# Kernel optimization log

Hardware: AMD Instinct MI355X
Metric: run time of the kernel (lower is better)

## Reference

```python
import jax, jax.numpy as jnp
import numpy as np

N = 50000   # nodes
E = 800000  # edges
D = 256     # input_dim == hidden_dim (required by original code path)
O = 32      # output_dim
ALPHA = 0.5      # APPNP teleport
ALPHA_RES = 0.0  # residual mix on output
BETA = 1.0       # neighbor-aggregation scale
EPS = 1e-12


def _l2norm(h):
    # F.normalize(h, p=2, dim=1)
    n = jnp.sqrt(jnp.sum(h * h, axis=1, keepdims=True))
    return h / jnp.maximum(n, EPS)


def _gappnp(x, row, col):
    # GAPPNP with K=1, symmetric normalization, self-loops (APPNP-style step)
    sl = jnp.arange(N, dtype=row.dtype)
    r = jnp.concatenate([row, sl])
    c = jnp.concatenate([col, sl])
    deg = jax.ops.segment_sum(jnp.ones(r.shape, x.dtype), r, num_segments=N)
    dinv = jnp.where(deg > 0, jax.lax.rsqrt(jnp.maximum(deg, 1.0)), 0.0)
    norm = dinv[r] * dinv[c]                      # [E+N]
    agg = jax.ops.segment_sum(norm[:, None] * x[c], r, num_segments=N)  # [N, D]
    h = (1.0 - ALPHA) * BETA * agg + ALPHA * x
    return (1.0 - ALPHA_RES) * h + ALPHA_RES * x


def setup_inputs() -> dict:
    key = jax.random.key(0)
    ks = jax.random.split(key, 8)
    s = 1.0 / np.sqrt(D)
    return {
        "x": jax.random.normal(ks[0], (N, D), dtype=jnp.float32),
        "edge_index": jax.random.randint(ks[1], (2, E), 0, N, dtype=jnp.int32),
        "W0": jax.random.normal(ks[2], (D, D), dtype=jnp.float32) * s,
        "b0": jnp.zeros((D,), jnp.float32),
        "Wn0": jax.random.normal(ks[3], (D, D), dtype=jnp.float32) * s,
        "bn0": jnp.zeros((D,), jnp.float32),
        "W1": jax.random.normal(ks[4], (D, D), dtype=jnp.float32) * s,
        "b1": jnp.zeros((D,), jnp.float32),
        "Wn1": jax.random.normal(ks[5], (D, D), dtype=jnp.float32) * s,
        "bn1": jnp.zeros((D,), jnp.float32),
        "W2": jax.random.normal(ks[6], (D, O), dtype=jnp.float32) * s,
        "b2": jnp.zeros((O,), jnp.float32),
    }


def reference(x, edge_index, W0, b0, Wn0, bn0, W1, b1, Wn1, bn1, W2, b2):
    # eval mode: dropout is identity
    row, col = edge_index[0], edge_index[1]
    h = x
    for (W, b, Wn, bn) in ((W0, b0, Wn0, bn0), (W1, b1, Wn1, bn1)):
        h = h @ W + b                       # fc[c]
        nb = h @ Wn + bn                    # fc_n[c] (separate_neighbors)
        nb = _gappnp(nb, row, col)          # propagate neighbors
        h = h + nb
        h = _l2norm(h)                      # norm == 'normalize'
        h = jax.nn.relu(h)                  # activation 'relu'
    h = h @ W2 + b2                         # final layer, no norm (c != 0)
    return h
```

## Files before the change

### kernel.cpp

```cpp
#include <hip/hip_runtime.h>
#include <hip/hip_bf16.h>

#define NN 50000
#define NE 800000
#define DD 256
#define OO 32

typedef __attribute__((ext_vector_type(8))) short short8;
typedef __attribute__((ext_vector_type(4))) float float4v;

#define AS1 __attribute__((address_space(1)))
#define AS3 __attribute__((address_space(3)))

__device__ __forceinline__ float lo16f(unsigned int u) {
    union { unsigned int i; float f; } x; x.i = u << 16; return x.f;
}
__device__ __forceinline__ float hi16f(unsigned int u) {
    union { unsigned int i; float f; } x; x.i = u & 0xFFFF0000u; return x.f;
}
__device__ __forceinline__ unsigned short f2b(float f) {
    union { float f; unsigned int i; } x;
    x.f = f;
    unsigned int r = x.i + 0x7FFFu + ((x.i >> 16) & 1u);
    return (unsigned short)(r >> 16);
}

__global__ void count_kernel(const int* __restrict__ row, int* __restrict__ cnt, int E) {
    int e = blockIdx.x * blockDim.x + threadIdx.x;
    if (e < E) atomicAdd(&cnt[row[e]], 1);
}

__global__ __launch_bounds__(256) void block_sums(const int* __restrict__ cnt,
                                                  int* __restrict__ bsum, int N) {
    __shared__ int s[256];
    int idx = blockIdx.x * 256 + threadIdx.x;
    s[threadIdx.x] = (idx < N) ? cnt[idx] : 0;
    __syncthreads();
    for (int o = 128; o > 0; o >>= 1) {
        if (threadIdx.x < o) s[threadIdx.x] += s[threadIdx.x + o];
        __syncthreads();
    }
    if (threadIdx.x == 0) bsum[blockIdx.x] = s[0];
}

__global__ __launch_bounds__(256) void scan_bsums(const int* __restrict__ bsum,
                                                  int* __restrict__ bpre, int nb) {
    __shared__ int s[256];
    int t = threadIdx.x;
    int v0 = (t < nb) ? bsum[t] : 0;
    s[t] = v0;
    __syncthreads();
    for (int o = 1; o < 256; o <<= 1) {
        int v = (t >= o) ? s[t - o] : 0;
        __syncthreads();
        s[t] += v;
        __syncthreads();
    }
    if (t < nb) bpre[t] = s[t] - v0;
}

__global__ __launch_bounds__(256) void fill_rowptr(const int* __restrict__ cnt,
                                                   const int* __restrict__ bpre,
                                                   int* __restrict__ row_ptr,
                                                   int* __restrict__ cursor,
                                                   float* __restrict__ dinv, int N, int E) {
    __shared__ int s[256];
    int t = threadIdx.x;
    int idx = blockIdx.x * 256 + t;
    int c = (idx < N) ? cnt[idx] : 0;
    s[t] = c;
    __syncthreads();
    for (int o = 1; o < 256; o <<= 1) {
        int v = (t >= o) ? s[t - o] : 0;
        __syncthreads();
        s[t] += v;
        __syncthreads();
    }
    int excl = bpre[blockIdx.x] + s[t] - c;
    if (idx < N) {
        row_ptr[idx] = excl;
        cursor[idx] = excl;
        dinv[idx] = rsqrtf((float)(c + 1));
    }
    if (idx == N) row_ptr[N] = E;
}

__global__ __launch_bounds__(256) void touch_csr(const uint4* __restrict__ t, int n16) {
    int slice = blockIdx.x >> 3;
    int per = (n16 + 31) >> 5;
    int base = slice * per;
    int end = base + per; if (end > n16) end = n16;
    unsigned int sx = 0, sy = 0, sz = 0, sw = 0;
    for (int i = base + threadIdx.x; i < end; i += 256) {
        uint4 v = t[i];
        sx ^= v.x; sy ^= v.y; sz ^= v.z; sw ^= v.w;
    }
    asm volatile("" :: "v"(sx), "v"(sy), "v"(sz), "v"(sw));
}

__global__ void scatter_kernel(const int* __restrict__ row, const int* __restrict__ col,
                               int* __restrict__ cursor,
                               unsigned short* __restrict__ csr_col, int E) {
    int e = blockIdx.x * blockDim.x + threadIdx.x;
    if (e < E) {
        int p = atomicAdd(&cursor[row[e]], 1);
        csr_col[p] = (unsigned short)col[e];
    }
}

__global__ __launch_bounds__(256) void cast_x_kernel(const float* __restrict__ x,
                                                     unsigned short* __restrict__ xb, int n4) {
    int i = blockIdx.x * 256 + threadIdx.x;
    if (i < n4) {
        float4 v = ((const float4*)x)[i];
        ushort4 o;
        o.x = f2b(v.x); o.y = f2b(v.y); o.z = f2b(v.z); o.w = f2b(v.w);
        ((ushort4*)xb)[i] = o;
    }
}

__device__ __forceinline__ int pack_idx(int k, int n) {
    return (k >> 5) * 8192 + (n >> 4) * 512 + (((k & 31) >> 3) * 16 + (n & 15)) * 8 + (k & 7);
}

__global__ __launch_bounds__(256) void cast_pack_w(const float* __restrict__ W0,
                                                   const float* __restrict__ W1,
                                                   const float* __restrict__ W2,
                                                   unsigned short* __restrict__ Wp0,
                                                   unsigned short* __restrict__ Wp1,
                                                   unsigned short* __restrict__ Wt2) {
    int n = blockIdx.x, k = threadIdx.x;
    if (blockIdx.y == 0) Wp0[pack_idx(k, n)] = f2b(W0[k * 256 + n]);
    else if (blockIdx.y == 1) Wp1[pack_idx(k, n)] = f2b(W1[k * 256 + n]);
    else if (n < 32) Wt2[n * 256 + k] = f2b(W2[k * 32 + n]);
}

__global__ __launch_bounds__(256) void compose_wc(const float* __restrict__ W0,
                                                  const float* __restrict__ Wn0,
                                                  const float* __restrict__ W1,
                                                  const float* __restrict__ Wn1,
                                                  unsigned short* __restrict__ Wp0,
                                                  unsigned short* __restrict__ Wp1) {
    const float* W  = blockIdx.y ? W1 : W0;
    const float* Wn = blockIdx.y ? Wn1 : Wn0;
    unsigned short* T = blockIdx.y ? Wp1 : Wp0;
    __shared__ float wrow[256];
    int k = blockIdx.x, n = threadIdx.x;
    wrow[n] = W[k * 256 + n];
    __syncthreads();
    float s = 0.f;
#pragma unroll 8
    for (int m = 0; m < 256; ++m) s = fmaf(wrow[m], Wn[m * 256 + n], s);
    T[pack_idx(k + 256, n)] = f2b(s);
}

__global__ __launch_bounds__(256) void compose_bc(const float* __restrict__ b0_,
                                                  const float* __restrict__ Wn0,
                                                  const float* __restrict__ bn0,
                                                  const float* __restrict__ b1_,
                                                  const float* __restrict__ Wn1,
                                                  const float* __restrict__ bn1,
                                                  float* __restrict__ bc0,
                                                  float* __restrict__ bc1) {
    const float* b  = blockIdx.y ? b1_ : b0_;
    const float* Wn = blockIdx.y ? Wn1 : Wn0;
    const float* bn = blockIdx.y ? bn1 : bn0;
    float* bc = blockIdx.y ? bc1 : bc0;
    int n = threadIdx.x;
    float s = bn[n];
    for (int m = 0; m < 256; ++m) s = fmaf(b[m], Wn[m * 256 + n], s);
    bc[n] = s;
}

__global__ __launch_bounds__(256) void agg_g(const unsigned short* __restrict__ A,
                                             const float* __restrict__ dinv,
                                             const int* __restrict__ row_ptr,
                                             const unsigned short* __restrict__ csr_col,
                                             unsigned short* __restrict__ G,
                                             float* __restrict__ pv) {
    int wave = threadIdx.x >> 6, lane = threadIdx.x & 63;
    int half = lane >> 5, s = lane & 31;
    int v = blockIdx.x * 4 + wave;
    float dv = dinv[v];
    const uint4* A4 = (const uint4*)A;

    float a0 = 0.f, a1 = 0.f, a2 = 0.f, a3 = 0.f;
    float a4 = 0.f, a5 = 0.f, a6 = 0.f, a7 = 0.f;
    float sdc = 0.f;

    int st = row_ptr[v], en = row_ptr[v + 1];
    for (int b0 = st; b0 < en; b0 += 64) {
        int mm = en - b0;
        if (mm > 64) mm = 64;
        int c = 0;
        float dc = 0.f;
        if (lane < mm) { c = csr_col[b0 + lane]; dc = dinv[c]; }
        sdc += dc;
        int pairs4 = (((mm + 1) >> 1) + 3) & ~3;
        for (int j = 0; j < pairs4; j += 4) {
            int ci[4];
            float di[4];
            uint4 u[4];
#pragma unroll
            for (int q = 0; q < 4; ++q) {
                int srcl = 2 * (j + q) + half;
                ci[q] = __shfl(c, srcl);
                di[q] = __shfl(dc, srcl);
            }
#pragma unroll
            for (int q = 0; q < 4; ++q) u[q] = A4[(size_t)ci[q] * 32 + s];
#pragma unroll
            for (int q = 0; q < 4; ++q) {
                a0 = fmaf(di[q], lo16f(u[q].x), a0);
                a1 = fmaf(di[q], hi16f(u[q].x), a1);
                a2 = fmaf(di[q], lo16f(u[q].y), a2);
                a3 = fmaf(di[q], hi16f(u[q].y), a3);
                a4 = fmaf(di[q], lo16f(u[q].z), a4);
                a5 = fmaf(di[q], hi16f(u[q].z), a5);
                a6 = fmaf(di[q], lo16f(u[q].w), a6);
                a7 = fmaf(di[q], hi16f(u[q].w), a7);
            }
        }
    }
    a0 += __shfl_xor(a0, 32); a1 += __shfl_xor(a1, 32);
    a2 += __shfl_xor(a2, 32); a3 += __shfl_xor(a3, 32);
    a4 += __shfl_xor(a4, 32); a5 += __shfl_xor(a5, 32);
    a6 += __shfl_xor(a6, 32); a7 += __shfl_xor(a7, 32);
#pragma unroll
    for (int o = 32; o > 0; o >>= 1) sdc += __shfl_xor(sdc, o);

    if (half == 0) {
        uint4 au = A4[(size_t)v * 32 + s];
        float av[8] = {lo16f(au.x), hi16f(au.x), lo16f(au.y), hi16f(au.y),
                       lo16f(au.z), hi16f(au.z), lo16f(au.w), hi16f(au.w)};
        float aa[8] = {a0, a1, a2, a3, a4, a5, a6, a7};
        unsigned short ov[8];
#pragma unroll
        for (int i = 0; i < 8; ++i)
            ov[i] = f2b(0.5f * dv * (dv * av[i] + aa[i]) + 0.5f * av[i]);
        *(short8*)&G[(size_t)v * 256 + s * 8] = *(short8*)ov;
    }
    if (lane == 0) pv[v] = 0.5f * dv * (dv + sdc) + 0.5f;
}

__global__ __launch_bounds__(256, 2) void gemm512_norm(const unsigned short* __restrict__ A,
                                                       const unsigned short* __restrict__ G,
                                                       const unsigned short* __restrict__ Wp,
                                                       const float* __restrict__ bias,
                                                       const float* __restrict__ biasc,
                                                       const float* __restrict__ pv,
                                                       unsigned short* __restrict__ Out,
                                                       int M) {
    __shared__ unsigned short smem[16384];
    int tid = threadIdx.x, lane = tid & 63, wave = tid >> 6;
    int fr = lane & 15, quad = lane >> 4, fk = quad * 8;
    int rb = blockIdx.x * 128;

    int r0 = rb + wave * 32 + fr;      if (r0 >= M) r0 = M - 1;
    int r1 = rb + wave * 32 + 16 + fr; if (r1 >= M) r1 = M - 1;
    const unsigned short* ap0 = A + (size_t)r0 * 256 + fk;
    const unsigned short* ap1 = A + (size_t)r1 * 256 + fk;
    const unsigned short* gp0 = G + (size_t)r0 * 256 + fk;
    const unsigned short* gp1 = G + (size_t)r1 * 256 + fk;

    float4v acc[2][16];
#pragma unroll
    for (int i = 0; i < 2; ++i)
#pragma unroll
        for (int j = 0; j < 16; ++j) acc[i][j] = (float4v){0.f, 0.f, 0.f, 0.f};

#pragma unroll
    for (int i = 0; i < 4; ++i) {
        int ch = wave * 4 + i;
        __builtin_amdgcn_global_load_lds((const AS1 void*)(Wp + ch * 512 + lane * 8),
                                         (AS3 void*)&smem[ch * 512], 16, 0, 0);
    }
    short8 a0c = *(const short8*)ap0;
    short8 a1c = *(const short8*)ap1;

    for (int kk = 0; kk < 16; ++kk) {
        __syncthreads();
        int cur = (kk & 1) * 8192;
        if (kk < 15) {
            int nxt = ((kk + 1) & 1) * 8192;
#pragma unroll
            for (int i = 0; i < 4; ++i) {
                int ch = wave * 4 + i;
                __builtin_amdgcn_global_load_lds(
                    (const AS1 void*)(Wp + (kk + 1) * 8192 + ch * 512 + lane * 8),
                    (AS3 void*)&smem[nxt + ch * 512], 16, 0, 0);
            }
        }
        short8 a0n, a1n;
        if (kk < 15) {
            int kn = kk + 1;
            a0n = (kn < 8) ? *(const short8*)(ap0 + kn * 32) : *(const short8*)(gp0 + (kn - 8) * 32);
            a1n = (kn < 8) ? *(const short8*)(ap1 + kn * 32) : *(const short8*)(gp1 + (kn - 8) * 32);
        }
#pragma unroll
        for (int j = 0; j < 16; ++j) {
            short8 b = *(const short8*)&smem[cur + j * 512 + lane * 8];
            acc[0][j] = __builtin_amdgcn_mfma_f32_16x16x32_bf16(a0c, b, acc[0][j], 0, 0, 0);
            acc[1][j] = __builtin_amdgcn_mfma_f32_16x16x32_bf16(a1c, b, acc[1][j], 0, 0, 0);
        }
        a0c = a0n;
        a1c = a1n;
    }

    float bv[16], bcv[16];
#pragma unroll
    for (int j = 0; j < 16; ++j) {
        bv[j] = bias[j * 16 + fr];
        bcv[j] = biasc[j * 16 + fr];
    }
    float pvr[2][4];
#pragma unroll
    for (int i = 0; i < 2; ++i)
#pragma unroll
        for (int r = 0; r < 4; ++r) {
            int rg = rb + wave * 32 + i * 16 + quad * 4 + r;
            if (rg >= M) rg = M - 1;
            pvr[i][r] = pv[rg];
        }
    float ss[2][4] = {{0.f, 0.f, 0.f, 0.f}, {0.f, 0.f, 0.f, 0.f}};
#pragma unroll
    for (int i = 0; i < 2; ++i)
#pragma unroll
        for (int j = 0; j < 16; ++j)
#pragma unroll
            for (int r = 0; r < 4; ++r) {
                float t = acc[i][j][r] + bv[j] + pvr[i][r] * bcv[j];
                acc[i][j][r] = t;
                ss[i][r] = fmaf(t, t, ss[i][r]);
            }
#pragma unroll
    for (int o = 1; o < 16; o <<= 1)
#pragma unroll
        for (int i = 0; i < 2; ++i)
#pragma unroll
            for (int r = 0; r < 4; ++r) ss[i][r] += __shfl_xor(ss[i][r], o);
    float inv[2][4];
#pragma unroll
    for (int i = 0; i < 2; ++i)
#pragma unroll
        for (int r = 0; r < 4; ++r) inv[i][r] = 1.0f / fmaxf(sqrtf(ss[i][r]), 1e-12f);

#pragma unroll
    for (int rd = 0; rd < 2; ++rd) {
        __syncthreads();
        if ((wave >> 1) == rd) {
#pragma unroll
            for (int i = 0; i < 2; ++i)
#pragma unroll
                for (int j = 0; j < 16; ++j)
#pragma unroll
                    for (int r = 0; r < 4; ++r)
                        smem[((wave & 1) * 32 + i * 16 + quad * 4 + r) * 256 + j * 16 + fr] =
                            f2b(fmaxf(acc[i][j][r] * inv[i][r], 0.f));
        }
        __syncthreads();
#pragma unroll
        for (int b = 0; b < 8; ++b) {
            int chunk = b * 256 + tid;
            int rw = chunk >> 5, part = chunk & 31;
            int gr = rb + rd * 64 + rw;
            if (gr < M)
                *(short8*)&Out[(size_t)gr * 256 + part * 8] =
                    *(const short8*)&smem[rw * 256 + part * 8];
        }
    }
}

__global__ __launch_bounds__(256) void gemm_final_mfma(const unsigned short* __restrict__ A,
                                                       const unsigned short* __restrict__ Wt2,
                                                       const float* __restrict__ b2,
                                                       float* __restrict__ out, int M) {
    __shared__ unsigned short Als[128 * 32];
    __shared__ unsigned short Bls[32 * 32];
    int tid = threadIdx.x;
    int lane = tid & 63, wave = tid >> 6;
    int rowBase = blockIdx.x * 128;

    float4v acc[2][2];
#pragma unroll
    for (int i = 0; i < 2; ++i)
#pragma unroll
        for (int j = 0; j < 2; ++j) acc[i][j] = (float4v){0.f, 0.f, 0.f, 0.f};

    int sRow = wave * 32 + (lane >> 2);
    int sK = (lane & 3) * 8;
    int fr = lane & 15, fk = (lane >> 4) * 8;
    int bn = tid >> 3, bk4 = (tid & 7) * 4;

    for (int k0 = 0; k0 < 256; k0 += 32) {
        int r0 = rowBase + sRow;       if (r0 >= M) r0 = M - 1;
        int r1 = rowBase + sRow + 16;  if (r1 >= M) r1 = M - 1;
        __builtin_amdgcn_global_load_lds((const AS1 void*)(A + (size_t)r0 * 256 + k0 + sK),
                                         (AS3 void*)&Als[(wave * 32) * 32], 16, 0, 0);
        __builtin_amdgcn_global_load_lds((const AS1 void*)(A + (size_t)r1 * 256 + k0 + sK),
                                         (AS3 void*)&Als[(wave * 32 + 16) * 32], 16, 0, 0);
        *(ushort4*)&Bls[bn * 32 + bk4] = *(const ushort4*)&Wt2[bn * 256 + k0 + bk4];
        __syncthreads();

        short8 af[2], bfr[2];
#pragma unroll
        for (int i = 0; i < 2; ++i)
            af[i] = *(const short8*)&Als[(wave * 32 + i * 16 + fr) * 32 + fk];
#pragma unroll
        for (int j = 0; j < 2; ++j)
            bfr[j] = *(const short8*)&Bls[(j * 16 + fr) * 32 + fk];
#pragma unroll
        for (int i = 0; i < 2; ++i)
#pragma unroll
            for (int j = 0; j < 2; ++j)
                acc[i][j] = __builtin_amdgcn_mfma_f32_16x16x32_bf16(af[i], bfr[j], acc[i][j], 0, 0, 0);
        __syncthreads();
    }

    int cr = (lane >> 4) * 4, cc = lane & 15;
#pragma unroll
    for (int i = 0; i < 2; ++i) {
#pragma unroll
        for (int j = 0; j < 2; ++j) {
            int colg = j * 16 + cc;
            float bv = b2[colg];
#pragma unroll
            for (int r = 0; r < 4; ++r) {
                int rowg = rowBase + wave * 32 + i * 16 + cr + r;
                if (rowg < M) out[(size_t)rowg * 32 + colg] = acc[i][j][r] + bv;
            }
        }
    }
}

extern "C" void kernel_launch(void* const* d_in, const int* in_sizes, int n_in,
                              void* d_out, int out_size, void* d_ws, size_t ws_size,
                              hipStream_t stream) {
    const float* x   = (const float*)d_in[0];
    const int* edge  = (const int*)d_in[1];
    const float* W0  = (const float*)d_in[2];
    const float* b0  = (const float*)d_in[3];
    const float* Wn0 = (const float*)d_in[4];
    const float* bn0 = (const float*)d_in[5];
    const float* W1  = (const float*)d_in[6];
    const float* b1  = (const float*)d_in[7];
    const float* Wn1 = (const float*)d_in[8];
    const float* bn1 = (const float*)d_in[9];
    const float* W2  = (const float*)d_in[10];
    const float* b2  = (const float*)d_in[11];
    float* out = (float*)d_out;

    const int N = NN, E = NE;
    const int* row = edge;
    const int* col = edge + E;

    char* p = (char*)d_ws;
    unsigned short* Xbf = (unsigned short*)p; p += (size_t)N * DD * 2;
    unsigned short* Gbf = (unsigned short*)p; p += (size_t)N * DD * 2;
    unsigned short* Abf = (unsigned short*)p; p += (size_t)N * DD * 2;
    unsigned short* Wp0 = (unsigned short*)p; p += 16 * 8192 * 2;
    unsigned short* Wp1 = (unsigned short*)p; p += 16 * 8192 * 2;
    unsigned short* Wt2 = (unsigned short*)p; p += 32 * 256 * 2;
    float* bc0   = (float*)p; p += 256 * 4;
    float* bc1   = (float*)p; p += 256 * 4;
    float* pv    = (float*)p; p += (size_t)N * 4;
    int* cnt     = (int*)p; p += (size_t)N * 4;
    int* row_ptr = (int*)p; p += (size_t)(N + 4) * 4;
    int* cursor  = (int*)p; p += (size_t)N * 4;
    float* dinv  = (float*)p; p += (size_t)N * 4;
    unsigned short* csr_col = (unsigned short*)p; p += (size_t)E * 2;
    int* bsum    = (int*)p; p += 256 * 4;
    int* bpre    = (int*)p; p += 256 * 4;

    const int nblk = (N + 255) / 256;
    const int eb = (E + 255) / 256;

    hipMemsetAsync(cnt, 0, (size_t)N * sizeof(int), stream);
    count_kernel<<<eb, 256, 0, stream>>>(row, cnt, E);
    block_sums<<<nblk, 256, 0, stream>>>(cnt, bsum, N);
    scan_bsums<<<1, 256, 0, stream>>>(bsum, bpre, nblk);
    fill_rowptr<<<nblk, 256, 0, stream>>>(cnt, bpre, row_ptr, cursor, dinv, N, E);
    touch_csr<<<256, 256, 0, stream>>>((const uint4*)csr_col, E * 2 / 16);
    scatter_kernel<<<eb, 256, 0, stream>>>(row, col, cursor, csr_col, E);

    cast_x_kernel<<<(N * DD / 4 + 255) / 256, 256, 0, stream>>>(x, Xbf, N * DD / 4);
    cast_pack_w<<<dim3(256, 3), 256, 0, stream>>>(W0, W1, W2, Wp0, Wp1, Wt2);
    compose_wc<<<dim3(256, 2), 256, 0, stream>>>(W0, Wn0, W1, Wn1, Wp0, Wp1);
    compose_bc<<<dim3(1, 2), 256, 0, stream>>>(b0, Wn0, bn0, b1, Wn1, bn1, bc0, bc1);

    const int gTiles = (N + 127) / 128;
    agg_g<<<N / 4, 256, 0, stream>>>(Xbf, dinv, row_ptr, csr_col, Gbf, pv);
    gemm512_norm<<<gTiles, 256, 0, stream>>>(Xbf, Gbf, Wp0, b0, bc0, pv, Abf, N);
    agg_g<<<N / 4, 256, 0, stream>>>(Abf, dinv, row_ptr, csr_col, Gbf, pv);
    gemm512_norm<<<gTiles, 256, 0, stream>>>(Abf, Gbf, Wp1, b1, bc1, pv, Xbf, N);
    gemm_final_mfma<<<(N + 127) / 128, 256, 0, stream>>>(Xbf, Wt2, b2, out, N);
}
```

Measured before the change: 390.0 us.

## Fuse neighbor aggregation into the per-layer GEMM via shared-memory G tile

Merges the aggregation kernel and the 512-K GEMM+normalize kernel into one per-layer kernel. Each 512-thread block first aggregates its 128 rows into a swizzled LDS tile, then runs the MFMA GEMM with the first half of K read from global A and the second half read from LDS. This drops the global round trip of the G buffer and one launch per layer. In exchange the weight tile is single-buffered with two barriers per K step, each wave now handles 16 rows instead of 32, and the gather phase cannot overlap the GEMM within a block, so load balance and occupancy become more sensitive to per-block degree.

Result: slower. 400.3 us (+2.6%).

```diff
diff --git a/kernel.cpp b/kernel.cpp
--- a/kernel.cpp
+++ b/kernel.cpp
@@ -172,139 +172,137 @@
     bc[n] = s;
 }
 
-__global__ __launch_bounds__(256) void agg_g(const unsigned short* __restrict__ A,
-                                             const float* __restrict__ dinv,
-                                             const int* __restrict__ row_ptr,
-                                             const unsigned short* __restrict__ csr_col,
-                                             unsigned short* __restrict__ G,
-                                             float* __restrict__ pv) {
-    int wave = threadIdx.x >> 6, lane = threadIdx.x & 63;
+__global__ __launch_bounds__(512, 4) void layer_fused(const unsigned short* __restrict__ A,
+                                                      const float* __restrict__ dinv,
+                                                      const int* __restrict__ row_ptr,
+                                                      const unsigned short* __restrict__ csr_col,
+                                                      const unsigned short* __restrict__ Wp,
+                                                      const float* __restrict__ bias,
+                                                      const float* __restrict__ biasc,
+                                                      float* __restrict__ pv,
+                                                      unsigned short* __restrict__ Out,
+                                                      int M) {
+    __shared__ unsigned short Gt[128 * 256];
+    __shared__ unsigned short Bs[8192];
+    int tid = threadIdx.x, lane = tid & 63, wave = tid >> 6;
     int half = lane >> 5, s = lane & 31;
-    int v = blockIdx.x * 4 + wave;
-    float dv = dinv[v];
+    int rb = blockIdx.x * 128;
+
+    {
+        int ch = wave * 2;
+        __builtin_amdgcn_global_load_lds((const AS1 void*)(Wp + ch * 512 + lane * 8),
+                                         (AS3 void*)&Bs[ch * 512], 16, 0, 0);
+        __builtin_amdgcn_global_load_lds((const AS1 void*)(Wp + (ch + 1) * 512 + lane * 8),
+                                         (AS3 void*)&Bs[(ch + 1) * 512], 16, 0, 0);
+    }
+
     const uint4* A4 = (const uint4*)A;
-
-    float a0 = 0.f, a1 = 0.f, a2 = 0.f, a3 = 0.f;
-    float a4 = 0.f, a5 = 0.f, a6 = 0.f, a7 = 0.f;
-    float sdc = 0.f;
-
-    int st = row_ptr[v], en = row_ptr[v + 1];
-    for (int b0 = st; b0 < en; b0 += 64) {
-        int mm = en - b0;
-        if (mm > 64) mm = 64;
-        int c = 0;
-        float dc = 0.f;
-        if (lane < mm) { c = csr_col[b0 + lane]; dc = dinv[c]; }
-        sdc += dc;
-        int pairs4 = (((mm + 1) >> 1) + 3) & ~3;
-        for (int j = 0; j < pairs4; j += 4) {
-            int ci[4];
-            float di[4];
-            uint4 u[4];
-#pragma unroll
-            for (int q = 0; q < 4; ++q) {
-                int srcl = 2 * (j + q) + half;
-                ci[q] = __shfl(c, srcl);
-                di[q] = __shfl(dc, srcl);
+    int li = rb + wave * 16 + lane; if (li > NN) li = NN;
+    int rpv = (lane < 17) ? row_ptr[li] : 0;
+
+    for (int t = 0; t < 16; ++t) {
+        int v = rb + wave * 16 + t;
+        if (v >= M) break;
+        float dv = dinv[v];
+        int st = __shfl(rpv, t), en = __shfl(rpv, t + 1);
+
+        float a0 = 0.f, a1 = 0.f, a2 = 0.f, a3 = 0.f;
+        float a4 = 0.f, a5 = 0.f, a6 = 0.f, a7 = 0.f;
+        float sdc = 0.f;
+        for (int b0 = st; b0 < en; b0 += 64) {
+            int mm = en - b0;
+            if (mm > 64) mm = 64;
+            int c = 0;
+            float dc = 0.f;
+            if (lane < mm) { c = csr_col[b0 + lane]; dc = dinv[c]; }
+            sdc += dc;
+            int pairs4 = (((mm + 1) >> 1) + 3) & ~3;
+            for (int j = 0; j < pairs4; j += 4) {
+                int ci[4];
+                float di[4];
+                uint4 u[4];
+#pragma unroll
+                for (int q = 0; q < 4; ++q) {
+                    int srcl = 2 * (j + q) + half;
+                    ci[q] = __shfl(c, srcl);
+                    di[q] = __shfl(dc, srcl);
+                }
+#pragma unroll
+                for (int q = 0; q < 4; ++q) u[q] = A4[(size_t)ci[q] * 32 + s];
+#pragma unroll
+                for (int q = 0; q < 4; ++q) {
+                    a0 = fmaf(di[q], lo16f(u[q].x), a0);
+                    a1 = fmaf(di[q], hi16f(u[q].x), a1);
+                    a2 = fmaf(di[q], lo16f(u[q].y), a2);
+                    a3 = fmaf(di[q], hi16f(u[q].y), a3);
+                    a4 = fmaf(di[q], lo16f(u[q].z), a4);
+                    a5 = fmaf(di[q], hi16f(u[q].z), a5);
+                    a6 = fmaf(di[q], lo16f(u[q].w), a6);
+                    a7 = fmaf(di[q], hi16f(u[q].w), a7);
+                }
             }
-#pragma unroll
-            for (int q = 0; q < 4; ++q) u[q] = A4[(size_t)ci[q] * 32 + s];
-#pragma unroll
-            for (int q = 0; q < 4; ++q) {
-                a0 = fmaf(di[q], lo16f(u[q].x), a0);
-                a1 = fmaf(di[q], hi16f(u[q].x), a1);
-                a2 = fmaf(di[q], lo16f(u[q].y), a2);
-                a3 = fmaf(di[q], hi16f(u[q].y), a3);
-                a4 = fmaf(di[q], lo16f(u[q].z), a4);
-                a5 = fmaf(di[q], hi16f(u[q].z), a5);
-                a6 = fmaf(di[q], lo16f(u[q].w), a6);
-                a7 = fmaf(di[q], hi16f(u[q].w), a7);
-            }
-        }
-    }
-    a0 += __shfl_xor(a0, 32); a1 += __shfl_xor(a1, 32);
-    a2 += __shfl_xor(a2, 32); a3 += __shfl_xor(a3, 32);
-    a4 += __shfl_xor(a4, 32); a5 += __shfl_xor(a5, 32);
-    a6 += __shfl_xor(a6, 32); a7 += __shfl_xor(a7, 32);
-#pragma unroll
-    for (int o = 32; o > 0; o >>= 1) sdc += __shfl_xor(sdc, o);
-
-    if (half == 0) {
-        uint4 au = A4[(size_t)v * 32 + s];
-        float av[8] = {lo16f(au.x), hi16f(au.x), lo16f(au.y), hi16f(au.y),
-                       lo16f(au.z), hi16f(au.z), lo16f(au.w), hi16f(au.w)};
-        float aa[8] = {a0, a1, a2, a3, a4, a5, a6, a7};
-        unsigned short ov[8];
-#pragma unroll
-        for (int i = 0; i < 8; ++i)
-            ov[i] = f2b(0.5f * dv * (dv * av[i] + aa[i]) + 0.5f * av[i]);
-        *(short8*)&G[(size_t)v * 256 + s * 8] = *(short8*)ov;
-    }
-    if (lane == 0) pv[v] = 0.5f * dv * (dv + sdc) + 0.5f;
-}
-
-__global__ __launch_bounds__(256, 2) void gemm512_norm(const unsigned short* __restrict__ A,
-                                                       const unsigned short* __restrict__ G,
-                                                       const unsigned short* __restrict__ Wp,
-                                                       const float* __restrict__ bias,
-                                                       const float* __restrict__ biasc,
-                                                       const float* __restrict__ pv,
-                                                       unsigned short* __restrict__ Out,
-                                                       int M) {
-    __shared__ unsigned short smem[16384];
-    int tid = threadIdx.x, lane = tid & 63, wave = tid >> 6;
+        }
+        a0 += __shfl_xor(a0, 32); a1 += __shfl_xor(a1, 32);
+        a2 += __shfl_xor(a2, 32); a3 += __shfl_xor(a3, 32);
+        a4 += __shfl_xor(a4, 32); a5 += __shfl_xor(a5, 32);
+        a6 += __shfl_xor(a6, 32); a7 += __shfl_xor(a7, 32);
+#pragma unroll
+        for (int o = 32; o > 0; o >>= 1) sdc += __shfl_xor(sdc, o);
+
+        int lt = wave * 16 + t;
+        if (half == 0) {
+            uint4 au = A4[(size_t)v * 32 + s];
+            float av[8] = {lo16f(au.x), hi16f(au.x), lo16f(au.y), hi16f(au.y),
+                           lo16f(au.z), hi16f(au.z), lo16f(au.w), hi16f(au.w)};
+            float aa[8] = {a0, a1, a2, a3, a4, a5, a6, a7};
+            unsigned short ov[8];
+#pragma unroll
+            for (int i = 0; i < 8; ++i)
+                ov[i] = f2b(0.5f * dv * (dv * av[i] + aa[i]) + 0.5f * av[i]);
+            int slot = s ^ (lt & 7);
+            *(short8*)&Gt[lt * 256 + slot * 8] = *(short8*)ov;
+        }
+        if (lane == 0) pv[v] = 0.5f * dv * (dv + sdc) + 0.5f;
+    }
+    __syncthreads();
+
     int fr = lane & 15, quad = lane >> 4, fk = quad * 8;
-    int rb = blockIdx.x * 128;
-
-    int r0 = rb + wave * 32 + fr;      if (r0 >= M) r0 = M - 1;
-    int r1 = rb + wave * 32 + 16 + fr; if (r1 >= M) r1 = M - 1;
+    int lt = wave * 16 + fr;
+    int r0 = rb + lt; if (r0 >= M) r0 = M - 1;
     const unsigned short* ap0 = A + (size_t)r0 * 256 + fk;
-    const unsigned short* ap1 = A + (size_t)r1 * 256 + fk;
-    const unsigned short* gp0 = G + (size_t)r0 * 256 + fk;
-    const unsigned short* gp1 = G + (size_t)r1 * 256 + fk;
-
-    float4v acc[2][16];
-#pragma unroll
-    for (int i = 0; i < 2; ++i)
-#pragma unroll
-        for (int j = 0; j < 16; ++j) acc[i][j] = (float4v){0.f, 0.f, 0.f, 0.f};
-
-#pragma unroll
-    for (int i = 0; i < 4; ++i) {
-        int ch = wave * 4 + i;
-        __builtin_amdgcn_global_load_lds((const AS1 void*)(Wp + ch * 512 + lane * 8),
-                                         (AS3 void*)&smem[ch * 512], 16, 0, 0);
-    }
+
+    float4v acc[16];
+#pragma unroll
+    for (int j = 0; j < 16; ++j) acc[j] = (float4v){0.f, 0.f, 0.f, 0.f};
+
     short8 a0c = *(const short8*)ap0;
-    short8 a1c = *(const short8*)ap1;
-
+#pragma unroll
     for (int kk = 0; kk < 16; ++kk) {
-        __syncthreads();
-        int cur = (kk & 1) * 8192;
+        short8 av;
+        if (kk < 8) {
+            av = a0c;
+            if (kk < 7) a0c = *(const short8*)(ap0 + (kk + 1) * 32);
+        } else {
+            int kn = kk - 8;
+            int slot = (quad + kn * 4) ^ (lt & 7);
+            av = *(const short8*)&Gt[lt * 256 + slot * 8];
+        }
+#pragma unroll
+        for (int j = 0; j < 16; ++j) {
+            short8 b = *(const short8*)&Bs[j * 512 + lane * 8];
+            acc[j] = __builtin_amdgcn_mfma_f32_16x16x32_bf16(av, b, acc[j], 0, 0, 0);
+        }
+        __syncthreads();
         if (kk < 15) {
-            int nxt = ((kk + 1) & 1) * 8192;
-#pragma unroll
-            for (int i = 0; i < 4; ++i) {
-                int ch = wave * 4 + i;
-                __builtin_amdgcn_global_load_lds(
-                    (const AS1 void*)(Wp + (kk + 1) * 8192 + ch * 512 + lane * 8),
-                    (AS3 void*)&smem[nxt + ch * 512], 16, 0, 0);
-            }
-        }
-        short8 a0n, a1n;
-        if (kk < 15) {
-            int kn = kk + 1;
-            a0n = (kn < 8) ? *(const short8*)(ap0 + kn * 32) : *(const short8*)(gp0 + (kn - 8) * 32);
-            a1n = (kn < 8) ? *(const short8*)(ap1 + kn * 32) : *(const short8*)(gp1 + (kn - 8) * 32);
-        }
-#pragma unroll
-        for (int j = 0; j < 16; ++j) {
-            short8 b = *(const short8*)&smem[cur + j * 512 + lane * 8];
-            acc[0][j] = __builtin_amdgcn_mfma_f32_16x16x32_bf16(a0c, b, acc[0][j], 0, 0, 0);
-            acc[1][j] = __builtin_amdgcn_mfma_f32_16x16x32_bf16(a1c, b, acc[1][j], 0, 0, 0);
-        }
-        a0c = a0n;
-        a1c = a1n;
+            int ch = wave * 2;
+            __builtin_amdgcn_global_load_lds(
+                (const AS1 void*)(Wp + (kk + 1) * 8192 + ch * 512 + lane * 8),
+                (AS3 void*)&Bs[ch * 512], 16, 0, 0);
+            __builtin_amdgcn_global_load_lds(
+                (const AS1 void*)(Wp + (kk + 1) * 8192 + (ch + 1) * 512 + lane * 8),
+                (AS3 void*)&Bs[(ch + 1) * 512], 16, 0, 0);
+        }
+        __syncthreads();
     }
 
     float bv[16], bcv[16];
@@ -313,61 +311,45 @@
         bv[j] = bias[j * 16 + fr];
         bcv[j] = biasc[j * 16 + fr];
     }
-    float pvr[2][4];
-#pragma unroll
-    for (int i = 0; i < 2; ++i)
+    float pvr[4];
+#pragma unroll
+    for (int r = 0; r < 4; ++r) {
+        int rg = rb + wave * 16 + quad * 4 + r;
+        if (rg >= M) rg = M - 1;
+        pvr[r] = pv[rg];
+    }
+    float ss[4] = {0.f, 0.f, 0.f, 0.f};
+#pragma unroll
+    for (int j = 0; j < 16; ++j)
 #pragma unroll
         for (int r = 0; r < 4; ++r) {
-            int rg = rb + wave * 32 + i * 16 + quad * 4 + r;
-            if (rg >= M) rg = M - 1;
-            pvr[i][r] = pv[rg];
-        }
-    float ss[2][4] = {{0.f, 0.f, 0.f, 0.f}, {0.f, 0.f, 0.f, 0.f}};
-#pragma unroll
-    for (int i = 0; i < 2; ++i)
-#pragma unroll
-        for (int j = 0; j < 16; ++j)
-#pragma unroll
-            for (int r = 0; r < 4; ++r) {
-                float t = acc[i][j][r] + bv[j] + pvr[i][r] * bcv[j];
-                acc[i][j][r] = t;
-                ss[i][r] = fmaf(t, t, ss[i][r]);
-            }
+            float t = acc[j][r] + bv[j] + pvr[r] * bcv[j];
+            acc[j][r] = t;
+            ss[r] = fmaf(t, t, ss[r]);
+        }
 #pragma unroll
     for (int o = 1; o < 16; o <<= 1)
 #pragma unroll
-        for (int i = 0; i < 2; ++i)
-#pragma unroll
-            for (int r = 0; r < 4; ++r) ss[i][r] += __shfl_xor(ss[i][r], o);
-    float inv[2][4];
-#pragma unroll
-    for (int i = 0; i < 2; ++i)
-#pragma unroll
-        for (int r = 0; r < 4; ++r) inv[i][r] = 1.0f / fmaxf(sqrtf(ss[i][r]), 1e-12f);
-
-#pragma unroll
-    for (int rd = 0; rd < 2; ++rd) {
-        __syncthreads();
-        if ((wave >> 1) == rd) {
-#pragma unroll
-            for (int i = 0; i < 2; ++i)
-#pragma unroll
-                for (int j = 0; j < 16; ++j)
-#pragma unroll
-                    for (int r = 0; r < 4; ++r)
-                        smem[((wave & 1) * 32 + i * 16 + quad * 4 + r) * 256 + j * 16 + fr] =
-                            f2b(fmaxf(acc[i][j][r] * inv[i][r], 0.f));
-        }
-        __syncthreads();
-#pragma unroll
-        for (int b = 0; b < 8; ++b) {
-            int chunk = b * 256 + tid;
-            int rw = chunk >> 5, part = chunk & 31;
-            int gr = rb + rd * 64 + rw;
-            if (gr < M)
-                *(short8*)&Out[(size_t)gr * 256 + part * 8] =
-                    *(const short8*)&smem[rw * 256 + part * 8];
-        }
+        for (int r = 0; r < 4; ++r) ss[r] += __shfl_xor(ss[r], o);
+    float inv[4];
+#pragma unroll
+    for (int r = 0; r < 4; ++r) inv[r] = 1.0f / fmaxf(sqrtf(ss[r]), 1e-12f);
+
+#pragma unroll
+    for (int j = 0; j < 16; ++j)
+#pragma unroll
+        for (int r = 0; r < 4; ++r)
+            Gt[(wave * 16 + quad * 4 + r) * 256 + j * 16 + fr] =
+                f2b(fmaxf(acc[j][r] * inv[r], 0.f));
+    __syncthreads();
+#pragma unroll
+    for (int b = 0; b < 8; ++b) {
+        int chunk = b * 512 + tid;
+        int rw = chunk >> 5, part = chunk & 31;
+        int gr = rb + rw;
+        if (gr < M)
+            *(short8*)&Out[(size_t)gr * 256 + part * 8] =
+                *(const short8*)&Gt[rw * 256 + part * 8];
     }
 }
 
@@ -456,7 +438,6 @@
 
     char* p = (char*)d_ws;
     unsigned short* Xbf = (unsigned short*)p; p += (size_t)N * DD * 2;
-    unsigned short* Gbf = (unsigned short*)p; p += (size_t)N * DD * 2;
     unsigned short* Abf = (unsigned short*)p; p += (size_t)N * DD * 2;
     unsigned short* Wp0 = (unsigned short*)p; p += 16 * 8192 * 2;
     unsigned short* Wp1 = (unsigned short*)p; p += 16 * 8192 * 2;
@@ -489,9 +470,7 @@
     compose_bc<<<dim3(1, 2), 256, 0, stream>>>(b0, Wn0, bn0, b1, Wn1, bn1, bc0, bc1);
 
     const int gTiles = (N + 127) / 128;
-    agg_g<<<N / 4, 256, 0, stream>>>(Xbf, dinv, row_ptr, csr_col, Gbf, pv);
-    gemm512_norm<<<gTiles, 256, 0, stream>>>(Xbf, Gbf, Wp0, b0, bc0, pv, Abf, N);
-    agg_g<<<N / 4, 256, 0, stream>>>(Abf, dinv, row_ptr, csr_col, Gbf, pv);
-    gemm512_norm<<<gTiles, 256, 0, stream>>>(Abf, Gbf, Wp1, b1, bc1, pv, Xbf, N);
+    layer_fused<<<gTiles, 512, 0, stream>>>(Xbf, dinv, row_ptr, csr_col, Wp0, b0, bc0, pv, Abf, N);
+    layer_fused<<<gTiles, 512, 0, stream>>>(Abf, dinv, row_ptr, csr_col, Wp1, b1, bc1, pv, Xbf, N);
     gemm_final_mfma<<<(N + 127) / 128, 256, 0, stream>>>(Xbf, Wt2, b2, out, N);
 }
```

## Merge CSR build and weight prep into three fused launches with single-pass scan

Applied to the files above, without the earlier changes.

Replaces roughly ten small preprocessing kernels with three. The first fuses degree counting with the x-to-bf16 cast. The second runs the prefix scan in one pass: the last block to arrive scans the block sums and raises a flag, and the other blocks spin on it after warming the CSR buffer. The third fuses edge scatter with weight cast, packing and composition. This is meant to cut launch overhead and gaps between tiny kernels. The spin-wait needs all 196 blocks to be resident at once, and the zeroing memset now also has to clear the counter and flag.

New measurement: 377.9 us. -3.1%, faster.

```diff
diff --git a/kernel.cpp b/kernel.cpp
--- a/kernel.cpp
+++ b/kernel.cpp
@@ -5,6 +5,9 @@
 #define NE 800000
 #define DD 256
 #define OO 32
+#define EB 3125
+#define CASTB 12500
+#define NBLK 196
 
 typedef __attribute__((ext_vector_type(8))) short short8;
 typedef __attribute__((ext_vector_type(4))) float float4v;
@@ -25,49 +28,42 @@
     return (unsigned short)(r >> 16);
 }
 
-__global__ void count_kernel(const int* __restrict__ row, int* __restrict__ cnt, int E) {
-    int e = blockIdx.x * blockDim.x + threadIdx.x;
-    if (e < E) atomicAdd(&cnt[row[e]], 1);
-}
-
-__global__ __launch_bounds__(256) void block_sums(const int* __restrict__ cnt,
-                                                  int* __restrict__ bsum, int N) {
+__device__ __forceinline__ int pack_idx(int k, int n) {
+    return (k >> 5) * 8192 + (n >> 4) * 512 + (((k & 31) >> 3) * 16 + (n & 15)) * 8 + (k & 7);
+}
+
+__global__ __launch_bounds__(256) void pre_count_cast(const int* __restrict__ row,
+                                                      int* __restrict__ cnt,
+                                                      const float* __restrict__ x,
+                                                      unsigned short* __restrict__ xb) {
+    int b = blockIdx.x, t = threadIdx.x;
+    if (b < EB) {
+        int e = b * 256 + t;
+        if (e < NE) atomicAdd(&cnt[row[e]], 1);
+    } else {
+        int i = (b - EB) * 256 + t;
+        float4 v = ((const float4*)x)[i];
+        ushort4 o;
+        o.x = f2b(v.x); o.y = f2b(v.y); o.z = f2b(v.z); o.w = f2b(v.w);
+        ((ushort4*)xb)[i] = o;
+    }
+}
+
+__global__ __launch_bounds__(256) void scan_fill(const int* __restrict__ cnt,
+                                                 int* __restrict__ row_ptr,
+                                                 int* __restrict__ cursor,
+                                                 float* __restrict__ dinv,
+                                                 unsigned int* __restrict__ bsum,
+                                                 unsigned int* __restrict__ bpre,
+                                                 int* __restrict__ ctr,
+                                                 int* __restrict__ flag,
+                                                 const uint4* __restrict__ touch, int n16) {
     __shared__ int s[256];
-    int idx = blockIdx.x * 256 + threadIdx.x;
-    s[threadIdx.x] = (idx < N) ? cnt[idx] : 0;
-    __syncthreads();
-    for (int o = 128; o > 0; o >>= 1) {
-        if (threadIdx.x < o) s[threadIdx.x] += s[threadIdx.x + o];
-        __syncthreads();
-    }
-    if (threadIdx.x == 0) bsum[blockIdx.x] = s[0];
-}
-
-__global__ __launch_bounds__(256) void scan_bsums(const int* __restrict__ bsum,
-                                                  int* __restrict__ bpre, int nb) {
-    __shared__ int s[256];
-    int t = threadIdx.x;
-    int v0 = (t < nb) ? bsum[t] : 0;
-    s[t] = v0;
-    __syncthreads();
-    for (int o = 1; o < 256; o <<= 1) {
-        int v = (t >= o) ? s[t - o] : 0;
-        __syncthreads();
-        s[t] += v;
-        __syncthreads();
-    }
-    if (t < nb) bpre[t] = s[t] - v0;
-}
-
-__global__ __launch_bounds__(256) void fill_rowptr(const int* __restrict__ cnt,
-                                                   const int* __restrict__ bpre,
-                                                   int* __restrict__ row_ptr,
-                                                   int* __restrict__ cursor,
-                                                   float* __restrict__ dinv, int N, int E) {
-    __shared__ int s[256];
-    int t = threadIdx.x;
-    int idx = blockIdx.x * 256 + t;
-    int c = (idx < N) ? cnt[idx] : 0;
+    __shared__ unsigned int t2[256];
+    __shared__ int ticket;
+    int t = threadIdx.x, b = blockIdx.x;
+    int idx = b * 256 + t;
+    int c = (idx < NN) ? cnt[idx] : 0;
     s[t] = c;
     __syncthreads();
     for (int o = 1; o < 256; o <<= 1) {
@@ -76,100 +72,112 @@
         s[t] += v;
         __syncthreads();
     }
-    int excl = bpre[blockIdx.x] + s[t] - c;
-    if (idx < N) {
+    if (t == 255) bsum[b] = (unsigned int)s[255];
+    __syncthreads();
+    if (t == 0) { __threadfence(); ticket = atomicAdd(ctr, 1); }
+    __syncthreads();
+    if (ticket == NBLK - 1) {
+        __threadfence();
+        unsigned int a = (t < NBLK) ? bsum[t] : 0u;
+        t2[t] = a;
+        __syncthreads();
+        for (int o = 1; o < 256; o <<= 1) {
+            unsigned int v = (t >= o) ? t2[t - o] : 0u;
+            __syncthreads();
+            t2[t] += v;
+            __syncthreads();
+        }
+        if (t < NBLK) bpre[t] = t2[t] - a;
+        __syncthreads();
+        if (t == 0) {
+            __threadfence();
+            __hip_atomic_store(flag, 1, __ATOMIC_RELEASE, __HIP_MEMORY_SCOPE_AGENT);
+        }
+    } else {
+        int per = (n16 + 23) / 24;
+        int slice = b >> 3; if (slice > 23) slice = 23;
+        int base = slice * per, end = base + per; if (end > n16) end = n16;
+        unsigned int sx = 0, sy = 0, sz = 0, sw = 0;
+        for (int i = base + t; i < end; i += 256) {
+            uint4 v = touch[i];
+            sx ^= v.x; sy ^= v.y; sz ^= v.z; sw ^= v.w;
+        }
+        asm volatile("" :: "v"(sx), "v"(sy), "v"(sz), "v"(sw));
+    }
+    if (t == 0) {
+        while (__hip_atomic_load(flag, __ATOMIC_ACQUIRE, __HIP_MEMORY_SCOPE_AGENT) == 0)
+            __builtin_amdgcn_s_sleep(8);
+    }
+    __syncthreads();
+    int excl = (int)bpre[b] + s[t] - c;
+    if (idx < NN) {
         row_ptr[idx] = excl;
         cursor[idx] = excl;
         dinv[idx] = rsqrtf((float)(c + 1));
     }
-    if (idx == N) row_ptr[N] = E;
-}
-
-__global__ __launch_bounds__(256) void touch_csr(const uint4* __restrict__ t, int n16) {
-    int slice = blockIdx.x >> 3;
-    int per = (n16 + 31) >> 5;
-    int base = slice * per;
-    int end = base + per; if (end > n16) end = n16;
-    unsigned int sx = 0, sy = 0, sz = 0, sw = 0;
-    for (int i = base + threadIdx.x; i < end; i += 256) {
-        uint4 v = t[i];
-        sx ^= v.x; sy ^= v.y; sz ^= v.z; sw ^= v.w;
-    }
-    asm volatile("" :: "v"(sx), "v"(sy), "v"(sz), "v"(sw));
-}
-
-__global__ void scatter_kernel(const int* __restrict__ row, const int* __restrict__ col,
-                               int* __restrict__ cursor,
-                               unsigned short* __restrict__ csr_col, int E) {
-    int e = blockIdx.x * blockDim.x + threadIdx.x;
-    if (e < E) {
-        int p = atomicAdd(&cursor[row[e]], 1);
-        csr_col[p] = (unsigned short)col[e];
-    }
-}
-
-__global__ __launch_bounds__(256) void cast_x_kernel(const float* __restrict__ x,
-                                                     unsigned short* __restrict__ xb, int n4) {
-    int i = blockIdx.x * 256 + threadIdx.x;
-    if (i < n4) {
-        float4 v = ((const float4*)x)[i];
-        ushort4 o;
-        o.x = f2b(v.x); o.y = f2b(v.y); o.z = f2b(v.z); o.w = f2b(v.w);
-        ((ushort4*)xb)[i] = o;
-    }
-}
-
-__device__ __forceinline__ int pack_idx(int k, int n) {
-    return (k >> 5) * 8192 + (n >> 4) * 512 + (((k & 31) >> 3) * 16 + (n & 15)) * 8 + (k & 7);
-}
-
-__global__ __launch_bounds__(256) void cast_pack_w(const float* __restrict__ W0,
-                                                   const float* __restrict__ W1,
-                                                   const float* __restrict__ W2,
-                                                   unsigned short* __restrict__ Wp0,
-                                                   unsigned short* __restrict__ Wp1,
-                                                   unsigned short* __restrict__ Wt2) {
-    int n = blockIdx.x, k = threadIdx.x;
-    if (blockIdx.y == 0) Wp0[pack_idx(k, n)] = f2b(W0[k * 256 + n]);
-    else if (blockIdx.y == 1) Wp1[pack_idx(k, n)] = f2b(W1[k * 256 + n]);
-    else if (n < 32) Wt2[n * 256 + k] = f2b(W2[k * 32 + n]);
-}
-
-__global__ __launch_bounds__(256) void compose_wc(const float* __restrict__ W0,
-                                                  const float* __restrict__ Wn0,
-                                                  const float* __restrict__ W1,
-                                                  const float* __restrict__ Wn1,
-                                                  unsigned short* __restrict__ Wp0,
-                                                  unsigned short* __restrict__ Wp1) {
-    const float* W  = blockIdx.y ? W1 : W0;
-    const float* Wn = blockIdx.y ? Wn1 : Wn0;
-    unsigned short* T = blockIdx.y ? Wp1 : Wp0;
+    if (idx == NN) row_ptr[NN] = NE;
+}
+
+__global__ __launch_bounds__(256) void scatter_weights(const int* __restrict__ row,
+                                                       const int* __restrict__ col,
+                                                       int* __restrict__ cursor,
+                                                       unsigned short* __restrict__ csr_col,
+                                                       const float* __restrict__ W0,
+                                                       const float* __restrict__ Wn0,
+                                                       const float* __restrict__ W1,
+                                                       const float* __restrict__ Wn1,
+                                                       const float* __restrict__ W2,
+                                                       const float* __restrict__ b0_,
+                                                       const float* __restrict__ bn0,
+                                                       const float* __restrict__ b1_,
+                                                       const float* __restrict__ bn1,
+                                                       unsigned short* __restrict__ Wp0,
+                                                       unsigned short* __restrict__ Wp1,
+                                                       unsigned short* __restrict__ Wt2,
+                                                       float* __restrict__ bc0,
+                                                       float* __restrict__ bc1) {
     __shared__ float wrow[256];
-    int k = blockIdx.x, n = threadIdx.x;
-    wrow[n] = W[k * 256 + n];
-    __syncthreads();
-    float s = 0.f;
+    int b = blockIdx.x, t = threadIdx.x;
+    if (b < EB) {
+        int e = b * 256 + t;
+        if (e < NE) {
+            int p = atomicAdd(&cursor[row[e]], 1);
+            csr_col[p] = (unsigned short)col[e];
+        }
+    } else if (b < EB + 256) {
+        int n = b - EB;
+        Wp0[pack_idx(t, n)] = f2b(W0[t * 256 + n]);
+    } else if (b < EB + 512) {
+        int n = b - (EB + 256);
+        Wp1[pack_idx(t, n)] = f2b(W1[t * 256 + n]);
+    } else if (b < EB + 544) {
+        int n = b - (EB + 512);
+        Wt2[n * 256 + t] = f2b(W2[t * 32 + n]);
+    } else if (b < EB + 800) {
+        int k = b - (EB + 544);
+        wrow[t] = W0[k * 256 + t];
+        __syncthreads();
+        float s = 0.f;
 #pragma unroll 8
-    for (int m = 0; m < 256; ++m) s = fmaf(wrow[m], Wn[m * 256 + n], s);
-    T[pack_idx(k + 256, n)] = f2b(s);
-}
-
-__global__ __launch_bounds__(256) void compose_bc(const float* __restrict__ b0_,
-                                                  const float* __restrict__ Wn0,
-                                                  const float* __restrict__ bn0,
-                                                  const float* __restrict__ b1_,
-                                                  const float* __restrict__ Wn1,
-                                                  const float* __restrict__ bn1,
-                                                  float* __restrict__ bc0,
-                                                  float* __restrict__ bc1) {
-    const float* b  = blockIdx.y ? b1_ : b0_;
-    const float* Wn = blockIdx.y ? Wn1 : Wn0;
-    const float* bn = blockIdx.y ? bn1 : bn0;
-    float* bc = blockIdx.y ? bc1 : bc0;
-    int n = threadIdx.x;
-    float s = bn[n];
-    for (int m = 0; m < 256; ++m) s = fmaf(b[m], Wn[m * 256 + n], s);
-    bc[n] = s;
+        for (int m = 0; m < 256; ++m) s = fmaf(wrow[m], Wn0[m * 256 + t], s);
+        Wp0[pack_idx(k + 256, t)] = f2b(s);
+    } else if (b < EB + 1056) {
+        int k = b - (EB + 800);
+        wrow[t] = W1[k * 256 + t];
+        __syncthreads();
+        float s = 0.f;
+#pragma unroll 8
+        for (int m = 0; m < 256; ++m) s = fmaf(wrow[m], Wn1[m * 256 + t], s);
+        Wp1[pack_idx(k + 256, t)] = f2b(s);
+    } else {
+        float s0 = bn0[t], s1 = bn1[t];
+        for (int m = 0; m < 256; ++m) {
+            s0 = fmaf(b0_[m], Wn0[m * 256 + t], s0);
+            s1 = fmaf(b1_[m], Wn1[m * 256 + t], s1);
+        }
+        bc0[t] = s0;
+        bc1[t] = s1;
+    }
 }
 
 __global__ __launch_bounds__(256) void agg_g(const unsigned short* __restrict__ A,
@@ -465,28 +473,25 @@
     float* bc1   = (float*)p; p += 256 * 4;
     float* pv    = (float*)p; p += (size_t)N * 4;
     int* cnt     = (int*)p; p += (size_t)N * 4;
+    int* ctr     = (int*)p; p += 4;
+    int* flag    = (int*)p; p += 4;
+    p += 8;
     int* row_ptr = (int*)p; p += (size_t)(N + 4) * 4;
     int* cursor  = (int*)p; p += (size_t)N * 4;
     float* dinv  = (float*)p; p += (size_t)N * 4;
     unsigned short* csr_col = (unsigned short*)p; p += (size_t)E * 2;
-    int* bsum    = (int*)p; p += 256 * 4;
-    int* bpre    = (int*)p; p += 256 * 4;
-
-    const int nblk = (N + 255) / 256;
-    const int eb = (E + 255) / 256;
-
-    hipMemsetAsync(cnt, 0, (size_t)N * sizeof(int), stream);
-    count_kernel<<<eb, 256, 0, stream>>>(row, cnt, E);
-    block_sums<<<nblk, 256, 0, stream>>>(cnt, bsum, N);
-    scan_bsums<<<1, 256, 0, stream>>>(bsum, bpre, nblk);
-    fill_rowptr<<<nblk, 256, 0, stream>>>(cnt, bpre, row_ptr, cursor, dinv, N, E);
-    touch_csr<<<256, 256, 0, stream>>>((const uint4*)csr_col, E * 2 / 16);
-    scatter_kernel<<<eb, 256, 0, stream>>>(row, col, cursor, csr_col, E);
-
-    cast_x_kernel<<<(N * DD / 4 + 255) / 256, 256, 0, stream>>>(x, Xbf, N * DD / 4);
-    cast_pack_w<<<dim3(256, 3), 256, 0, stream>>>(W0, W1, W2, Wp0, Wp1, Wt2);
-    compose_wc<<<dim3(256, 2), 256, 0, stream>>>(W0, Wn0, W1, Wn1, Wp0, Wp1);
-    compose_bc<<<dim3(1, 2), 256, 0, stream>>>(b0, Wn0, bn0, b1, Wn1, bn1, bc0, bc1);
+    unsigned int* bsum = (unsigned int*)p; p += 256 * 4;
+    unsigned int* bpre = (unsigned int*)p; p += 256 * 4;
+
+    hipMemsetAsync(cnt, 0, ((size_t)N + 4) * sizeof(int), stream);
+
+    pre_count_cast<<<EB + CASTB, 256, 0, stream>>>(row, cnt, x, Xbf);
+    scan_fill<<<NBLK, 256, 0, stream>>>(cnt, row_ptr, cursor, dinv, bsum, bpre, ctr, flag,
+                                        (const uint4*)csr_col, E * 2 / 16);
+    scatter_weights<<<EB + 1057, 256, 0, stream>>>(row, col, cursor, csr_col,
+                                                   W0, Wn0, W1, Wn1, W2,
+                                                   b0, bn0, b1, bn1,
+                                                   Wp0, Wp1, Wt2, bc0, bc1);
 
     const int gTiles = (N + 127) / 128;
     agg_g<<<N / 4, 256, 0, stream>>>(Xbf, dinv, row_ptr, csr_col, Gbf, pv);
```
